# Kernel optimization log

Hardware: AMD Instinct MI355X
Metric: run time of the kernel (lower is better)

## Reference

```python
import jax, jax.numpy as jnp
import numpy as np


def setup_inputs() -> dict:
    key = jax.random.key(0)
    k1, k2 = jax.random.split(key)
    B, I, O = 16384, 1024, 4096
    return {
        "input": jax.random.normal(k1, (B, I), dtype=jnp.float32),
        "centers": jax.random.normal(k2, (O, I), dtype=jnp.float32),
        "log_sigma": jnp.zeros((O,), dtype=jnp.float32),
    }


def reference(input, centers, log_sigma):
    # as the torch broadcast-subtract-square-sum, without the (B,O,I) intermediate)
    x_sq = jnp.sum(input * input, axis=-1, keepdims=True)        # [B, 1]
    c_sq = jnp.sum(centers * centers, axis=-1)                   # [O]
    cross = input @ centers.T                                     # [B, O]
    d2 = jnp.maximum(x_sq + c_sq[None, :] - 2.0 * cross, 0.0)     # [B, O]
    sigma = jnp.exp(log_sigma)                                    # [O]
    return jnp.exp(-d2 / (2.0 * sigma * sigma)[None, :])
```

## Files before the change

### kernel.cpp

```cpp
#include <hip/hip_runtime.h>
#include <hip/hip_bf16.h>
#include <stdint.h>

#define TM 16384
#define TN 4096
#define TK 1024

#define NT (TK / 64)

typedef __attribute__((ext_vector_type(8))) short bf16x8;
typedef __attribute__((ext_vector_type(4))) float f32x4;

static __device__ __forceinline__ ushort f2bf(float x) {
    __hip_bfloat16 h = __float2bfloat16(x);
    return *reinterpret_cast<ushort*>(&h);
}

__global__ __launch_bounds__(256) void rowsq_cvt(const float* __restrict__ src,
                                                 ushort* __restrict__ dst,
                                                 float* __restrict__ sq) {
    const int row = blockIdx.x;
    const int t = threadIdx.x;
    const size_t base = (size_t)row * TK + (size_t)t * 4;
    const float4 v = *(const float4*)(src + base);
    float s = v.x * v.x + v.y * v.y + v.z * v.z + v.w * v.w;

    ushort4 b;
    b.x = f2bf(v.x); b.y = f2bf(v.y); b.z = f2bf(v.z); b.w = f2bf(v.w);
    *(ushort4*)(dst + base) = b;

#pragma unroll
    for (int off = 32; off > 0; off >>= 1) s += __shfl_down(s, off);

    __shared__ float red[4];
    const int lane = t & 63, wave = t >> 6;
    if (lane == 0) red[wave] = s;
    __syncthreads();
    if (t == 0) sq[row] = red[0] + red[1] + red[2] + red[3];
}

__global__ __launch_bounds__(256) void scale_k(const float* __restrict__ ls,
                                               float* __restrict__ f) {
    const int i = blockIdx.x * 256 + threadIdx.x;
    if (i < TN) f[i] = -0.5f * expf(-2.0f * ls[i]);
}


#define STAGE(PAN, G, T, H) do {                                               \
    __builtin_amdgcn_global_load_lds(                                          \
        (const __attribute__((address_space(1))) void*)((G) + (size_t)(H) * 128 * TK + (size_t)(T) * 64), \
        (__attribute__((address_space(3))) void*)((PAN) + (H) * 8192 + wbase), \
        16, 0, 0);                                                             \
    __builtin_amdgcn_global_load_lds(                                          \
        (const __attribute__((address_space(1))) void*)((G) + (size_t)(H) * 128 * TK + 64 * TK + (size_t)(T) * 64), \
        (__attribute__((address_space(3))) void*)((PAN) + (H) * 8192 + 4096 + wbase), \
        16, 0, 0);                                                             \
} while (0)

#define READA(PAN, QM) do {                                                    \
    const ushort* _p = (PAN) + (size_t)(rowA + (QM) * 64) * 64 + cX;           \
    _Pragma("unroll") for (int _i = 0; _i < 4; ++_i)                           \
    _Pragma("unroll") for (int _k = 0; _k < 2; ++_k)                           \
        af[_i][_k] = *(const bf16x8*)(_p + _i * 1024 + _k * 32);               \
} while (0)

#define READB(PAN, QN) do {                                                    \
    const ushort* _p = (PAN) + (size_t)(rowB + (QN) * 32) * 64 + cX;           \
    _Pragma("unroll") for (int _n = 0; _n < 2; ++_n)                           \
    _Pragma("unroll") for (int _k = 0; _k < 2; ++_k)                           \
        bf[(QN) * 2 + _n][_k] = *(const bf16x8*)(_p + _n * 1024 + _k * 32);    \
} while (0)

#define MFMA16(QM, QN)                                                         \
    _Pragma("unroll") for (int _i = 0; _i < 4; ++_i)                           \
    _Pragma("unroll") for (int _n = 0; _n < 2; ++_n)                           \
    _Pragma("unroll") for (int _k = 0; _k < 2; ++_k)                           \
        acc[(QM) * 4 + _i][(QN) * 2 + _n] =                                    \
            __builtin_amdgcn_mfma_f32_16x16x32_bf16(                           \
                af[_i][_k], bf[(QN) * 2 + _n][_k],                             \
                acc[(QM) * 4 + _i][(QN) * 2 + _n], 0, 0, 0)

#define PH_SYNC do {                                                           \
    __builtin_amdgcn_s_barrier();                                              \
    asm volatile("s_waitcnt lgkmcnt(0)" ::: "memory");                         \
    __builtin_amdgcn_sched_barrier(0);                                         \
    __builtin_amdgcn_s_setprio(1);                                             \
} while (0)

#define PH_END do {                                                            \
    __builtin_amdgcn_s_setprio(0);                                             \
    __builtin_amdgcn_s_barrier();                                              \
} while (0)

#define PH_END_VM do {                                                         \
    __builtin_amdgcn_s_setprio(0);                                             \
    asm volatile("s_waitcnt vmcnt(4)" ::: "memory");                           \
    __builtin_amdgcn_s_barrier();                                              \
} while (0)

__global__ __launch_bounds__(512) void rbf_gemm(const ushort* __restrict__ A,
                                                const ushort* __restrict__ B,
                                                const float* __restrict__ xsq,
                                                const float* __restrict__ csq,
                                                const float* __restrict__ fsc,
                                                float* __restrict__ out) {
    __shared__ __align__(16) ushort lds[65536];

    const int bid = blockIdx.x;
    const int wg = (bid & 7) * 128 + (bid >> 3);
    const int bm = wg >> 4;
    const int bn = wg & 15;
    const int row0 = bm * 256;
    const int col0 = bn * 256;

    const int tid = threadIdx.x;
    const int lane = tid & 63, wave = tid >> 6;
    const int wr = wave >> 2, wc = wave & 3;
    const int lrow = lane & 15, lhi = lane >> 4;
    const int cX = (lhi * 8) ^ ((lrow & 4) << 2);
    const int rowA = wr * 128 + lrow;
    const int rowB = wc * 64 + lrow;
    const int wbase = wave * 512;

    const int srow = tid >> 3;
    const int scol = ((tid & 7) * 8) ^ ((tid & 32) >> 1);
    const ushort* gAl = A + (size_t)(row0 + srow) * TK + scol;
    const ushort* gBl = B + (size_t)(col0 + srow) * TK + scol;

    ushort* pA0 = lds;
    ushort* pB0 = lds + 16384;
    ushort* pA1 = lds + 32768;
    ushort* pB1 = lds + 49152;

    f32x4 acc[8][4];
#pragma unroll
    for (int m = 0; m < 8; ++m)
#pragma unroll
        for (int n = 0; n < 4; ++n)
            acc[m][n] = (f32x4){0.f, 0.f, 0.f, 0.f};

    bf16x8 af[4][2];
    bf16x8 bf[4][2];

    STAGE(pB0, gBl, 0, 0); STAGE(pB0, gBl, 0, 1);
    STAGE(pA0, gAl, 0, 0); STAGE(pA0, gAl, 0, 1);
    STAGE(pB1, gBl, 1, 0); STAGE(pB1, gBl, 1, 1);
    asm volatile("s_waitcnt vmcnt(4)" ::: "memory");
    __builtin_amdgcn_s_barrier();

#pragma unroll 1
    for (int t = 0; t < NT; t += 2) {
        const int T2 = (t + 2) & (NT - 1);
        const int T3 = (t + 3) & (NT - 1);

        READA(pA0, 0); READB(pB0, 0);
        STAGE(pA1, gAl, t + 1, 0);
        PH_SYNC; MFMA16(0, 0); PH_END;
        READB(pB0, 1);
        STAGE(pA1, gAl, t + 1, 1);
        PH_SYNC; MFMA16(0, 1); PH_END;
        READA(pA0, 1);
        STAGE(pB0, gBl, T2, 0);
        PH_SYNC; MFMA16(1, 0); PH_END;
        STAGE(pB0, gBl, T2, 1);
        PH_SYNC; MFMA16(1, 1); PH_END_VM;

        READA(pA1, 0); READB(pB1, 0);
        STAGE(pA0, gAl, T2, 0);
        PH_SYNC; MFMA16(0, 0); PH_END;
        READB(pB1, 1);
        STAGE(pA0, gAl, T2, 1);
        PH_SYNC; MFMA16(0, 1); PH_END;
        READA(pA1, 1);
        STAGE(pB1, gBl, T3, 0);
        PH_SYNC; MFMA16(1, 0); PH_END;
        STAGE(pB1, gBl, T3, 1);
        PH_SYNC; MFMA16(1, 1); PH_END_VM;
    }

    const int orow0 = row0 + wr * 128;
    const int ocol0 = col0 + wc * 64;
    float csv[4], fsv[4];
    int cidx[4];
#pragma unroll
    for (int n = 0; n < 4; ++n) {
        const int c = ocol0 + n * 16 + lrow;
        cidx[n] = c;
        csv[n] = csq[c];
        fsv[n] = fsc[c];
    }
#pragma unroll
    for (int m = 0; m < 8; ++m) {
        const int rb = orow0 + m * 16 + lhi * 4;
        const float4 xs = *(const float4*)(xsq + rb);
        const float xv[4] = {xs.x, xs.y, xs.z, xs.w};
#pragma unroll
        for (int n = 0; n < 4; ++n) {
#pragma unroll
            for (int j = 0; j < 4; ++j) {
                float d2 = fmaxf(xv[j] + csv[n] - 2.0f * acc[m][n][j], 0.0f);
                out[(size_t)(rb + j) * TN + cidx[n]] = __expf(fsv[n] * d2);
            }
        }
    }
}

extern "C" void kernel_launch(void* const* d_in, const int* in_sizes, int n_in,
                              void* d_out, int out_size, void* d_ws, size_t ws_size,
                              hipStream_t stream) {
    const float* inp = (const float*)d_in[0];
    const float* ctr = (const float*)d_in[1];
    const float* ls  = (const float*)d_in[2];
    float* out = (float*)d_out;

    ushort* Abf = (ushort*)d_ws;
    ushort* Bbf = Abf + (size_t)TM * TK;
    float* xsq = (float*)(Bbf + (size_t)TN * TK);
    float* csq = xsq + TM;
    float* fsc = csq + TN;

    rowsq_cvt<<<TM, 256, 0, stream>>>(inp, Abf, xsq);
    rowsq_cvt<<<TN, 256, 0, stream>>>(ctr, Bbf, csq);
    scale_k<<<(TN + 255) / 256, 256, 0, stream>>>(ls, fsc);

    rbf_gemm<<<(TM / 256) * (TN / 256), 512, 0, stream>>>(Abf, Bbf, xsq, csq, fsc, out);
}
```

Before: 185.1 us.

## Make GEMM persistent over four column tiles with continuous prefetch pipeline

The launch now uses 256 workgroups. Each one computes four consecutive 256-column output tiles for its row block, and the global-to-LDS prefetch runs across tile boundaries, so there is no cold pipeline start per tile. The LDS swizzle gains another XOR bit to reduce bank conflicts, and input loads and output stores use nontemporal hints. The price is fewer workgroups than CUs' worth of independent tiles, so the epilogue of one tile is serialised with the next tile's MFMAs. The load balance across 256 CUs also changes.

```diff
diff --git a/kernel.cpp b/kernel.cpp
--- a/kernel.cpp
+++ b/kernel.cpp
@@ -7,6 +7,7 @@
 #define TK 1024
 
 #define NT (TK / 64)
+#define JT 4
 
 typedef __attribute__((ext_vector_type(8))) short bf16x8;
 typedef __attribute__((ext_vector_type(4))) float f32x4;
@@ -22,7 +23,7 @@
     const int row = blockIdx.x;
     const int t = threadIdx.x;
     const size_t base = (size_t)row * TK + (size_t)t * 4;
-    const float4 v = *(const float4*)(src + base);
+    const f32x4 v = __builtin_nontemporal_load((const f32x4*)(src + base));
     float s = v.x * v.x + v.y * v.y + v.z * v.z + v.w * v.w;
 
     ushort4 b;
@@ -46,29 +47,32 @@
 }
 
 
-#define STAGE(PAN, G, T, H) do {                                               \
+#define STAGE(PAN, SRC, H) do {                                                \
     __builtin_amdgcn_global_load_lds(                                          \
-        (const __attribute__((address_space(1))) void*)((G) + (size_t)(H) * 128 * TK + (size_t)(T) * 64), \
+        (const __attribute__((address_space(1))) void*)((SRC) + (size_t)(H) * 128 * TK), \
         (__attribute__((address_space(3))) void*)((PAN) + (H) * 8192 + wbase), \
         16, 0, 0);                                                             \
     __builtin_amdgcn_global_load_lds(                                          \
-        (const __attribute__((address_space(1))) void*)((G) + (size_t)(H) * 128 * TK + 64 * TK + (size_t)(T) * 64), \
+        (const __attribute__((address_space(1))) void*)((SRC) + (size_t)(H) * 128 * TK + 64 * TK), \
         (__attribute__((address_space(3))) void*)((PAN) + (H) * 8192 + 4096 + wbase), \
         16, 0, 0);                                                             \
 } while (0)
 
+#define ASRC(S) (gAl + (size_t)((S) & 15) * 64)
+#define BSRC(S) (gBl + (size_t)(((S) & 63) >> 4) * (256 * (size_t)TK) + (size_t)((S) & 15) * 64)
+
 #define READA(PAN, QM) do {                                                    \
-    const ushort* _p = (PAN) + (size_t)(rowA + (QM) * 64) * 64 + cX;           \
     _Pragma("unroll") for (int _i = 0; _i < 4; ++_i)                           \
     _Pragma("unroll") for (int _k = 0; _k < 2; ++_k)                           \
-        af[_i][_k] = *(const bf16x8*)(_p + _i * 1024 + _k * 32);               \
+        af[_i][_k] = *(const bf16x8*)((PAN) +                                  \
+            (size_t)(rowA + (QM) * 64 + _i * 16) * 64 + (cX ^ (_k * 32)));     \
 } while (0)
 
 #define READB(PAN, QN) do {                                                    \
-    const ushort* _p = (PAN) + (size_t)(rowB + (QN) * 32) * 64 + cX;           \
     _Pragma("unroll") for (int _n = 0; _n < 2; ++_n)                           \
     _Pragma("unroll") for (int _k = 0; _k < 2; ++_k)                           \
-        bf[(QN) * 2 + _n][_k] = *(const bf16x8*)(_p + _n * 1024 + _k * 32);    \
+        bf[(QN) * 2 + _n][_k] = *(const bf16x8*)((PAN) +                       \
+            (size_t)(rowB + (QN) * 32 + _n * 16) * 64 + (cX ^ (_k * 32)));     \
 } while (0)
 
 #define MFMA16(QM, QN)                                                         \
@@ -107,99 +111,108 @@
     __shared__ __align__(16) ushort lds[65536];
 
     const int bid = blockIdx.x;
-    const int wg = (bid & 7) * 128 + (bid >> 3);
-    const int bm = wg >> 4;
-    const int bn = wg & 15;
+    const int wg = (bid & 7) * 32 + (bid >> 3);
+    const int bm = wg >> 2;
+    const int bnBase = (wg & 3) * 4;
     const int row0 = bm * 256;
-    const int col0 = bn * 256;
 
     const int tid = threadIdx.x;
     const int lane = tid & 63, wave = tid >> 6;
     const int wr = wave >> 2, wc = wave & 3;
     const int lrow = lane & 15, lhi = lane >> 4;
-    const int cX = (lhi * 8) ^ ((lrow & 4) << 2);
+    const int cX = (lhi * 8) ^ ((lrow & 4) << 2) ^ ((lrow & 8) << 2);
     const int rowA = wr * 128 + lrow;
     const int rowB = wc * 64 + lrow;
     const int wbase = wave * 512;
 
     const int srow = tid >> 3;
-    const int scol = ((tid & 7) * 8) ^ ((tid & 32) >> 1);
+    const int scol = ((tid & 7) * 8) ^ ((tid & 32) >> 1) ^ ((tid & 64) >> 1);
     const ushort* gAl = A + (size_t)(row0 + srow) * TK + scol;
-    const ushort* gBl = B + (size_t)(col0 + srow) * TK + scol;
+    const ushort* gBl = B + (size_t)(bnBase * 256 + srow) * TK + scol;
 
     ushort* pA0 = lds;
     ushort* pB0 = lds + 16384;
     ushort* pA1 = lds + 32768;
     ushort* pB1 = lds + 49152;
 
-    f32x4 acc[8][4];
-#pragma unroll
-    for (int m = 0; m < 8; ++m)
-#pragma unroll
-        for (int n = 0; n < 4; ++n)
-            acc[m][n] = (f32x4){0.f, 0.f, 0.f, 0.f};
-
     bf16x8 af[4][2];
     bf16x8 bf[4][2];
 
-    STAGE(pB0, gBl, 0, 0); STAGE(pB0, gBl, 0, 1);
-    STAGE(pA0, gAl, 0, 0); STAGE(pA0, gAl, 0, 1);
-    STAGE(pB1, gBl, 1, 0); STAGE(pB1, gBl, 1, 1);
+    STAGE(pB0, BSRC(0), 0); STAGE(pB0, BSRC(0), 1);
+    STAGE(pA0, ASRC(0), 0); STAGE(pA0, ASRC(0), 1);
+    STAGE(pB1, BSRC(1), 0); STAGE(pB1, BSRC(1), 1);
     asm volatile("s_waitcnt vmcnt(4)" ::: "memory");
     __builtin_amdgcn_s_barrier();
 
 #pragma unroll 1
-    for (int t = 0; t < NT; t += 2) {
-        const int T2 = (t + 2) & (NT - 1);
-        const int T3 = (t + 3) & (NT - 1);
-
-        READA(pA0, 0); READB(pB0, 0);
-        STAGE(pA1, gAl, t + 1, 0);
-        PH_SYNC; MFMA16(0, 0); PH_END;
-        READB(pB0, 1);
-        STAGE(pA1, gAl, t + 1, 1);
-        PH_SYNC; MFMA16(0, 1); PH_END;
-        READA(pA0, 1);
-        STAGE(pB0, gBl, T2, 0);
-        PH_SYNC; MFMA16(1, 0); PH_END;
-        STAGE(pB0, gBl, T2, 1);
-        PH_SYNC; MFMA16(1, 1); PH_END_VM;
-
-        READA(pA1, 0); READB(pB1, 0);
-        STAGE(pA0, gAl, T2, 0);
-        PH_SYNC; MFMA16(0, 0); PH_END;
-        READB(pB1, 1);
-        STAGE(pA0, gAl, T2, 1);
-        PH_SYNC; MFMA16(0, 1); PH_END;
-        READA(pA1, 1);
-        STAGE(pB1, gBl, T3, 0);
-        PH_SYNC; MFMA16(1, 0); PH_END;
-        STAGE(pB1, gBl, T3, 1);
-        PH_SYNC; MFMA16(1, 1); PH_END_VM;
-    }
-
-    const int orow0 = row0 + wr * 128;
-    const int ocol0 = col0 + wc * 64;
-    float csv[4], fsv[4];
-    int cidx[4];
-#pragma unroll
-    for (int n = 0; n < 4; ++n) {
-        const int c = ocol0 + n * 16 + lrow;
-        cidx[n] = c;
-        csv[n] = csq[c];
-        fsv[n] = fsc[c];
-    }
-#pragma unroll
-    for (int m = 0; m < 8; ++m) {
-        const int rb = orow0 + m * 16 + lhi * 4;
-        const float4 xs = *(const float4*)(xsq + rb);
-        const float xv[4] = {xs.x, xs.y, xs.z, xs.w};
+    for (int j = 0; j < JT; ++j) {
+        f32x4 acc[8][4];
+#pragma unroll
+        for (int m = 0; m < 8; ++m)
+#pragma unroll
+            for (int n = 0; n < 4; ++n)
+                acc[m][n] = (f32x4){0.f, 0.f, 0.f, 0.f};
+
+#pragma unroll 1
+        for (int t = 0; t < NT; t += 2) {
+            const int s = j * NT + t;
+
+            READA(pA0, 0); READB(pB0, 0);
+            STAGE(pA1, ASRC(s + 1), 0);
+            PH_SYNC; MFMA16(0, 0); PH_END;
+
+            READB(pB0, 1);
+            STAGE(pA1, ASRC(s + 1), 1);
+            PH_SYNC; MFMA16(0, 1); PH_END;
+
+            READA(pA0, 1);
+            STAGE(pB0, BSRC(s + 2), 0);
+            PH_SYNC; MFMA16(1, 0); PH_END;
+
+            STAGE(pB0, BSRC(s + 2), 1);
+            PH_SYNC; MFMA16(1, 1); PH_END_VM;
+
+            READA(pA1, 0); READB(pB1, 0);
+            STAGE(pA0, ASRC(s + 2), 0);
+            PH_SYNC; MFMA16(0, 0); PH_END;
+
+            READB(pB1, 1);
+            STAGE(pA0, ASRC(s + 2), 1);
+            PH_SYNC; MFMA16(0, 1); PH_END;
+
+            READA(pA1, 1);
+            STAGE(pB1, BSRC(s + 3), 0);
+            PH_SYNC; MFMA16(1, 0); PH_END;
+
+            STAGE(pB1, BSRC(s + 3), 1);
+            PH_SYNC; MFMA16(1, 1); PH_END_VM;
+        }
+
+        const int orow0 = row0 + wr * 128;
+        const int ocol0 = (bnBase + j) * 256 + wc * 64;
+        float csv[4], fsv[4];
+        int cidx[4];
 #pragma unroll
         for (int n = 0; n < 4; ++n) {
-#pragma unroll
-            for (int j = 0; j < 4; ++j) {
-                float d2 = fmaxf(xv[j] + csv[n] - 2.0f * acc[m][n][j], 0.0f);
-                out[(size_t)(rb + j) * TN + cidx[n]] = __expf(fsv[n] * d2);
+            const int c = ocol0 + n * 16 + lrow;
+            cidx[n] = c;
+            csv[n] = csq[c];
+            fsv[n] = fsc[c];
+        }
+#pragma unroll
+        for (int m = 0; m < 8; ++m) {
+            const int rb = orow0 + m * 16 + lhi * 4;
+            const f32x4 xs = *(const f32x4*)(xsq + rb);
+            const float xv[4] = {xs.x, xs.y, xs.z, xs.w};
+#pragma unroll
+            for (int n = 0; n < 4; ++n) {
+#pragma unroll
+                for (int jj = 0; jj < 4; ++jj) {
+                    float d2 = fmaxf(xv[jj] + csv[n] - 2.0f * acc[m][n][jj], 0.0f);
+                    const float v = __expf(fsv[n] * d2);
+                    __builtin_nontemporal_store(
+                        v, out + (size_t)(rb + jj) * TN + cidx[n]);
+                }
             }
         }
     }
@@ -223,5 +236,5 @@
     rowsq_cvt<<<TN, 256, 0, stream>>>(ctr, Bbf, csq);
     scale_k<<<(TN + 255) / 256, 256, 0, stream>>>(ls, fsc);
 
-    rbf_gemm<<<(TM / 256) * (TN / 256), 512, 0, stream>>>(Abf, Bbf, xsq, csq, fsc, out);
-}
+    rbf_gemm<<<256, 512, 0, stream>>>(Abf, Bbf, xsq, csq, fsc, out);
+}
```

Result: slower. 218.0 us (+17.8%).
